# Performance work log

Hardware: AMD Instinct MI355X
Metric: run time of the kernel (lower is better)

## Reference

```python
import jax, jax.numpy as jnp
import numpy as np

EPS = 1e-5
HD = 16          # hidden_dim
OC = 256         # out_chs
NH = 8           # num_heads (groups of qkv conv)
DV = OC // (2 * HD)  # per-head value dim = 8


def conv_bn_silu(x, w, gamma, beta, mean, var, stride=1, pad=1, groups=1):
    # Conv2d(bias=False) + BatchNorm2d(eval) + SiLU, NCHW/OIHW
    y = jax.lax.conv_general_dilated(
        x, w, (stride, stride), [(pad, pad), (pad, pad)],
        dimension_numbers=('NCHW', 'OIHW', 'NCHW'),
        feature_group_count=groups)
    inv = gamma * jax.lax.rsqrt(var + EPS)
    y = y * inv[None, :, None, None] + (beta - mean * inv)[None, :, None, None]
    return y * jax.nn.sigmoid(y)


def _bn_params(key, c):
    k1, k2, k3, k4 = jax.random.split(key, 4)
    g = 1.0 + 0.1 * jax.random.normal(k1, (c,), jnp.float32)
    b = 0.1 * jax.random.normal(k2, (c,), jnp.float32)
    m = 0.1 * jax.random.normal(k3, (c,), jnp.float32)
    v = jax.random.uniform(k4, (c,), jnp.float32, 0.5, 1.5)
    return g, b, m, v


def setup_inputs() -> dict:
    key = jax.random.key(0)
    ks = jax.random.split(key, 8)
    B, C, H, W = 16, 256, 80, 80
    qkv_out = HD * 2 + OC // 2  # 160
    d = {}
    d['x'] = jax.random.normal(ks[0], (B, C, H, W), jnp.float32)
    # qkv_conv: grouped 3x3, groups=NH -> in per group = C//NH
    d['qkv_w'] = jax.random.normal(ks[1], (qkv_out, C // NH, 3, 3), jnp.float32) * 0.05
    d['qkv_g'], d['qkv_b'], d['qkv_m'], d['qkv_v'] = _bn_params(ks[2], qkv_out)
    # hidden_conv: dense 3x3
    d['hid_w'] = jax.random.normal(ks[3], (OC, C, 3, 3), jnp.float32) * 0.02
    d['hid_g'], d['hid_b'], d['hid_m'], d['hid_v'] = _bn_params(ks[4], OC)
    # out_conv: 1x1 on (OC//2*3) channels
    d['out_w'] = jax.random.normal(ks[5], (OC, OC // 2 * 3, 1, 1), jnp.float32) * 0.05
    d['out_g'], d['out_b'], d['out_m'], d['out_v'] = _bn_params(ks[6], OC)
    return d


def reference(x, qkv_w, qkv_g, qkv_b, qkv_m, qkv_v,
              hid_w, hid_g, hid_b, hid_m, hid_v,
              out_w, out_g, out_b, out_m, out_v):
    B, C, H, W = x.shape
    N = H * W
    qkv = conv_bn_silu(x, qkv_w, qkv_g, qkv_b, qkv_m, qkv_v, stride=1, pad=1, groups=NH)
    q = qkv[:, :HD]               # (B, HD, H, W)
    k = qkv[:, HD:2 * HD]
    v = qkv[:, 2 * HD:]           # (B, OC//2, H, W)
    # permute to (B, N, HD) / (B, N, HD, DV), channel-major reshape matches torch .view
    q = q.transpose(0, 2, 3, 1).reshape(B, N, HD)
    k = k.transpose(0, 2, 3, 1).reshape(B, N, HD)
    v = v.transpose(0, 2, 3, 1).reshape(B, N, HD, DV)
    # per-pixel tiny attention: attn[b,n,i,j] = softmax_j(q_i * k_j)
    attn = jax.nn.softmax(q[..., :, None] * k[..., None, :], axis=-1)  # (B,N,HD,HD)
    y = jnp.einsum('bnij,bnjd->bnid', attn, v)                          # (B,N,HD,DV)
    # torch: permute(0,2,3,1).view(B, OC//2, H, W)
    y = y.transpose(0, 2, 3, 1).reshape(B, OC // 2, H, W)
    h = conv_bn_silu(x, hid_w, hid_g, hid_b, hid_m, hid_v, stride=1, pad=1)
    y = jnp.concatenate([y, h], axis=1)  # (B, OC//2*3, H, W)
    return conv_bn_silu(y, out_w, out_g, out_b, out_m, out_v, stride=1, pad=0)
```

## Files before the change

kernel.cpp:

```cpp
#include <hip/hip_runtime.h>
#include <stdint.h>

typedef unsigned short u16;
typedef unsigned int u32;
typedef __attribute__((ext_vector_type(4))) float f32x4;
typedef __attribute__((ext_vector_type(8))) __bf16 bf16x8;

#define EPS_BN 1e-5f

__device__ __forceinline__ u16 f2bf(float f) {
  u32 u = __builtin_bit_cast(u32, f);
  u32 r = (u + 0x7fffu + ((u >> 16) & 1u)) >> 16;
  return (u16)r;
}

__device__ __forceinline__ float silu_f(float v) {
  return v / (1.0f + __expf(-v));
}

__device__ __forceinline__ void gll16(const void* g, void* l) {
  __builtin_amdgcn_global_load_lds(
      (__attribute__((address_space(1))) void*)(void*)g,
      (__attribute__((address_space(3))) void*)l, 16, 0, 0);
}

__global__ __launch_bounds__(256) void prep(
    const float* __restrict__ qkv_w, const float* __restrict__ qg,
    const float* __restrict__ qb, const float* __restrict__ qm,
    const float* __restrict__ qv,
    const float* __restrict__ hid_w, const float* __restrict__ hg,
    const float* __restrict__ hb, const float* __restrict__ hm,
    const float* __restrict__ hv,
    const float* __restrict__ out_w, const float* __restrict__ og,
    const float* __restrict__ ob, const float* __restrict__ om,
    const float* __restrict__ ov,
    u16* __restrict__ wtb, u16* __restrict__ w2b, u16* __restrict__ wqp,
    float* __restrict__ bnq_s, float* __restrict__ bnq_b,
    float* __restrict__ bnh_s, float* __restrict__ bnh_b,
    float* __restrict__ bn2s, float* __restrict__ bn2b,
    float* __restrict__ zpg)
{
  const int gid = blockIdx.x * 256 + threadIdx.x;
  if (gid < 256 * 2304) {
    int j = gid / 2304, k = gid - j * 2304;
    int tap = k >> 8, c = k & 255;
    wtb[gid] = f2bf(hid_w[(j * 256 + c) * 9 + tap]);
  }
  if (gid < 73728) {
    int g = gid / 9216;
    int r = gid - g * 9216;
    int j = r / 288, k = r - j * 288;
    int tap = k >> 5, cg = k & 31;
    float v = 0.f;
    if (j < 20) v = qkv_w[((g * 20 + j) * 32 + cg) * 9 + tap];
    wqp[gid] = f2bf(v);
  }
  if (gid < 98304) w2b[gid] = f2bf(out_w[gid]);
  if (gid < 160) {
    float iv = qg[gid] * rsqrtf(qv[gid] + EPS_BN);
    bnq_s[gid] = iv; bnq_b[gid] = qb[gid] - qm[gid] * iv;
  }
  if (gid < 256) {
    float iv = hg[gid] * rsqrtf(hv[gid] + EPS_BN);
    bnh_s[gid] = iv; bnh_b[gid] = hb[gid] - hm[gid] * iv;
    float iv2 = og[gid] * rsqrtf(ov[gid] + EPS_BN);
    bn2s[gid] = iv2; bn2b[gid] = ob[gid] - om[gid] * iv2;
  }
  if (gid < 64) zpg[gid] = 0.f;
}

__global__ __launch_bounds__(256) void nchw2nhwc(
    const float* __restrict__ x, u16* __restrict__ xn)
{
  __shared__ u16 T[80 * 66];
  const int t = threadIdx.x;
  const int ct = blockIdx.x;
  const int h  = blockIdx.y;
  const int b  = blockIdx.z;
  const float* src = x + ((size_t)b * 256 + ct * 64) * 6400 + h * 80;
  for (int it = 0; it < 5; ++it) {
    int idx = it * 256 + t;
    int cl = idx / 20, w4 = idx - cl * 20;
    float4 v = *(const float4*)(src + (size_t)cl * 6400 + w4 * 4);
    T[(w4 * 4 + 0) * 66 + cl] = f2bf(v.x);
    T[(w4 * 4 + 1) * 66 + cl] = f2bf(v.y);
    T[(w4 * 4 + 2) * 66 + cl] = f2bf(v.z);
    T[(w4 * 4 + 3) * 66 + cl] = f2bf(v.w);
  }
  __syncthreads();
  u16* dst = xn + ((size_t)(b * 80 + h) * 80) * 256 + ct * 64;
  for (int it = 0; it < 5; ++it) {
    int idx = it * 256 + t;
    int wl = idx >> 4;
    int cl = (idx & 15) * 4;
    ushort4 v4;
    v4.x = T[wl * 66 + cl + 0];
    v4.y = T[wl * 66 + cl + 1];
    v4.z = T[wl * 66 + cl + 2];
    v4.w = T[wl * 66 + cl + 3];
    *(ushort4*)(dst + (size_t)wl * 256 + cl) = v4;
  }
}

__global__ __launch_bounds__(256, 2) void gemm_main(
    const u16* __restrict__ xn, const u16* __restrict__ wt,
    const float* __restrict__ bns, const float* __restrict__ bnb,
    const float* __restrict__ zpg, u16* __restrict__ ycat)
{
  __shared__ __attribute__((aligned(16))) u16 Al[128 * 64];
  __shared__ __attribute__((aligned(16))) u16 Bl[128 * 64];
  const int t = threadIdx.x;
  const int wave = t >> 6, lane = t & 63;
  const int wr = wave >> 1, wc = wave & 1;
  const int orig = blockIdx.y * 2 + blockIdx.x;
  const int wg = (orig & 7) * 200 + (orig >> 3);
  const int jtile = (wg / 800) * 128;
  const int ptile = (wg % 800) * 128;

  const int srcc = (((lane & 7) ^ ((lane >> 3) & 7)) * 8);
  int pb[4], hh[4], wwv[4], bofB[4];
#pragma unroll
  for (int c = 0; c < 4; ++c) {
    int m = wave * 32 + c * 8 + (lane >> 3);
    int p = ptile + m;
    pb[c] = p;
    int hw = p % 6400;
    hh[c] = hw / 80;
    wwv[c] = hw - (hw / 80) * 80;
    bofB[c] = (jtile + m) * 2304 + srcc;
  }
  u16* AlW = Al + wave * 2048;
  u16* BlW = Bl + wave * 2048;

  f32x4 acc[4][4];
#pragma unroll
  for (int m = 0; m < 4; ++m)
#pragma unroll
    for (int n = 0; n < 4; ++n) {
      f32x4 z = {0.f, 0.f, 0.f, 0.f};
      acc[m][n] = z;
    }

  for (int ks = 0; ks < 36; ++ks) {
    const int k0 = ks * 64;
    const int tap = k0 >> 8;
    const int c0 = k0 & 255;
    const int dh = tap / 3 - 1, dw = tap - (tap / 3) * 3 - 1;
    __syncthreads();
#pragma unroll
    for (int c = 0; c < 4; ++c) {
      int h2 = hh[c] + dh, w2 = wwv[c] + dw;
      bool ok = ((unsigned)h2 < 80u) & ((unsigned)w2 < 80u);
      const u16* src = ok
          ? (xn + ((size_t)(pb[c] + dh * 80 + dw) * 256 + c0 + srcc))
          : (const u16*)zpg;
      gll16(src, AlW + c * 512);
    }
#pragma unroll
    for (int c = 0; c < 4; ++c)
      gll16(wt + (size_t)(bofB[c] + k0), BlW + c * 512);
    __syncthreads();
#pragma unroll
    for (int kk = 0; kk < 2; ++kk) {
      const int q = kk * 4 + (lane >> 4);
      const int c16 = lane & 15;
      bf16x8 av[4], bv[4];
#pragma unroll
      for (int m = 0; m < 4; ++m) {
        int r = wr * 64 + m * 16 + c16;
        av[m] = *(const bf16x8*)(Al + r * 64 + (q ^ (r & 7)) * 8);
      }
#pragma unroll
      for (int n = 0; n < 4; ++n) {
        int r = wc * 64 + n * 16 + c16;
        bv[n] = *(const bf16x8*)(Bl + r * 64 + (q ^ (r & 7)) * 8);
      }
#pragma unroll
      for (int m = 0; m < 4; ++m)
#pragma unroll
        for (int n = 0; n < 4; ++n)
          acc[m][n] = __builtin_amdgcn_mfma_f32_16x16x32_bf16(
              av[m], bv[n], acc[m][n], 0, 0, 0);
    }
  }

  const int c16 = lane & 15, rg = lane >> 4;
#pragma unroll
  for (int n = 0; n < 4; ++n) {
    int j = jtile + wc * 64 + n * 16 + c16;
    float sc = bns[j], bi = bnb[j];
#pragma unroll
    for (int m = 0; m < 4; ++m) {
      int p0 = ptile + wr * 64 + m * 16 + rg * 4;
#pragma unroll
      for (int r = 0; r < 4; ++r) {
        float v = silu_f(acc[m][n][r] * sc + bi);
        ycat[(size_t)(p0 + r) * 384 + 128 + j] = f2bf(v);
      }
    }
  }
}

__global__ __launch_bounds__(256, 2) void qkv_attn(
    const u16* __restrict__ xn, const u16* __restrict__ wqp,
    const float* __restrict__ bnq_s, const float* __restrict__ bnq_b,
    u16* __restrict__ ycat)
{
  __shared__ __attribute__((aligned(16))) char LB[81920];
  u16* HB0 = (u16*)LB;
  u16* HB1 = (u16*)(LB + 40960);
  float* qs = (float*)LB;

  const int t = threadIdx.x;
  const int wave = t >> 6, lane = t & 63;
  const int orig = blockIdx.x;
  const int wg = (orig & 7) * 100 + (orig >> 3);
  const int ptile = wg * 128;
  const int pbase = ptile - 88;

  const int srcc = (((lane & 7) ^ ((lane >> 3) & 7)) * 8);
  const int q = lane >> 4, c16 = lane & 15;

  int ph[2], pw[2];
#pragma unroll
  for (int m = 0; m < 2; ++m) {
    int p = ptile + wave * 32 + m * 16 + c16;
    int hw = p % 6400;
    ph[m] = hw / 80;
    pw[m] = hw - (hw / 80) * 80;
  }

  auto STAGE_H = [&](int cc, u16* dst) {
#pragma unroll
    for (int r = 0; r < 10; ++r) {
      int row = r * 32 + wave * 8 + (lane >> 3);
      int p = pbase + row;
      int pc = p < 0 ? 0 : (p > 102399 ? 102399 : p);
      gll16(xn + (size_t)pc * 256 + cc * 64 + srcc,
            dst + (r * 32 + wave * 8) * 64);
    }
  };

  bf16x8 zv;
#pragma unroll
  for (int i = 0; i < 8; ++i) zv[i] = (__bf16)0.0f;

  f32x4 acc[2][16];
#pragma unroll
  for (int m = 0; m < 2; ++m)
#pragma unroll
    for (int f = 0; f < 16; ++f) {
      f32x4 z = {0.f, 0.f, 0.f, 0.f};
      acc[m][f] = z;
    }

  STAGE_H(0, HB0);
  asm volatile("s_waitcnt vmcnt(0)" ::: "memory");
  __builtin_amdgcn_sched_barrier(0);
  __syncthreads();

#pragma unroll
  for (int cc = 0; cc < 4; ++cc) {
    const u16* HBc = (cc & 1) ? HB1 : HB0;
    u16* HBn = (cc & 1) ? HB0 : HB1;
    if (cc < 3) STAGE_H(cc + 1, HBn);
    for (int tap = 0; tap < 9; ++tap) {
      const int dh = tap / 3 - 1, dw = tap - (tap / 3) * 3 - 1;
      const int dp = dh * 80 + dw;
      bf16x8 bq[2][2];
#pragma unroll
      for (int h = 0; h < 2; ++h)
#pragma unroll
        for (int nf = 0; nf < 2; ++nf) {
          int row = (2 * cc + h) * 32 + nf * 16 + c16;
          bq[h][nf] =
              *(const bf16x8*)(wqp + (size_t)row * 288 + tap * 32 + q * 8);
        }
      bf16x8 av[2][2];
#pragma unroll
      for (int m = 0; m < 2; ++m) {
        int rl = wave * 32 + m * 16 + c16 + 88 + dp;
        bool ok = ((unsigned)(ph[m] + dh) < 80u) &
                  ((unsigned)(pw[m] + dw) < 80u);
#pragma unroll
        for (int h = 0; h < 2; ++h) {
          int q8 = h * 4 + q;
          bf16x8 raw = *(const bf16x8*)(HBc + rl * 64 + ((q8 ^ (rl & 7)) * 8));
          av[m][h] = ok ? raw : zv;
        }
      }
#pragma unroll
      for (int h = 0; h < 2; ++h)
#pragma unroll
        for (int m = 0; m < 2; ++m)
#pragma unroll
          for (int nf = 0; nf < 2; ++nf)
            acc[m][(2 * cc + h) * 2 + nf] = __builtin_amdgcn_mfma_f32_16x16x32_bf16(
                av[m][h], bq[h][nf], acc[m][(2 * cc + h) * 2 + nf], 0, 0, 0);
    }
    if (cc < 3) {
      asm volatile("s_waitcnt vmcnt(0)" ::: "memory");
      __builtin_amdgcn_sched_barrier(0);
      __syncthreads();
    }
  }

  asm volatile("s_waitcnt vmcnt(0)" ::: "memory");
  __builtin_amdgcn_sched_barrier(0);
  __syncthreads();

#pragma unroll
  for (int f = 0; f < 16; ++f) {
    int jj = (f & 1) * 16 + c16;
    if (jj >= 20) continue;
    int oc = (f >> 1) * 20 + jj;
    float sc = bnq_s[oc], bi = bnq_b[oc];
#pragma unroll
    for (int m = 0; m < 2; ++m) {
      int pl0 = wave * 32 + m * 16 + q * 4;
#pragma unroll
      for (int r = 0; r < 4; ++r)
        qs[(pl0 + r) * 160 + oc] = silu_f(acc[m][f][r] * sc + bi);
    }
  }
  __syncthreads();

  for (int it = 0; it < 8; ++it) {
    int idx = it * 256 + t;
    int px = idx >> 4, i = idx & 15;
    const float* row = qs + px * 160;
    const float qi = row[i];
    float s[16];
    float mx = -3.4e38f;
#pragma unroll
    for (int j = 0; j < 16; ++j) { s[j] = qi * row[16 + j]; mx = fmaxf(mx, s[j]); }
    float sum = 0.f;
#pragma unroll
    for (int j = 0; j < 16; ++j) { s[j] = __expf(s[j] - mx); sum += s[j]; }
    const float inv = 1.0f / sum;
    float y[8];
#pragma unroll
    for (int d = 0; d < 8; ++d) y[d] = 0.f;
#pragma unroll
    for (int j = 0; j < 16; ++j) {
      const float a = s[j];
      const float* vr = row + 32 + j * 8;
#pragma unroll
      for (int d = 0; d < 8; ++d) y[d] += a * vr[d];
    }
    union { u16 u[8]; uint4 v4; } pk;
#pragma unroll
    for (int d = 0; d < 8; ++d) pk.u[d] = f2bf(y[d] * inv);
    *(uint4*)(ycat + (size_t)(ptile + px) * 384 + i * 8) = pk.v4;
  }
}

__global__ __launch_bounds__(256, 2) void gemm_out(
    const u16* __restrict__ w2, const u16* __restrict__ ycat,
    const float* __restrict__ bns, const float* __restrict__ bnb,
    float* __restrict__ out)
{
  __shared__ __attribute__((aligned(16))) u16 Al[128 * 64];
  __shared__ __attribute__((aligned(16))) u16 Bl[128 * 64];
  const int t = threadIdx.x;
  const int wave = t >> 6, lane = t & 63;
  const int wr = wave >> 1, wc = wave & 1;
  const int orig = blockIdx.y * 2 + blockIdx.x;
  const int wg = (orig & 7) * 200 + (orig >> 3);
  const int octile = (wg / 800) * 128;
  const int ptile = (wg % 800) * 128;

  const int srcc = (((lane & 7) ^ ((lane >> 3) & 7)) * 8);
  int bofA[4], bofB[4];
#pragma unroll
  for (int c = 0; c < 4; ++c) {
    int m = wave * 32 + c * 8 + (lane >> 3);
    bofA[c] = (octile + m) * 384 + srcc;
    bofB[c] = (ptile + m) * 384 + srcc;
  }
  u16* AlW = Al + wave * 2048;
  u16* BlW = Bl + wave * 2048;

  f32x4 acc[4][4];
#pragma unroll
  for (int m = 0; m < 4; ++m)
#pragma unroll
    for (int n = 0; n < 4; ++n) {
      f32x4 z = {0.f, 0.f, 0.f, 0.f};
      acc[m][n] = z;
    }

  for (int ks = 0; ks < 6; ++ks) {
    const int k0 = ks * 64;
    __syncthreads();
#pragma unroll
    for (int c = 0; c < 4; ++c) gll16(w2 + (size_t)(bofA[c] + k0), AlW + c * 512);
#pragma unroll
    for (int c = 0; c < 4; ++c) gll16(ycat + (size_t)(bofB[c] + k0), BlW + c * 512);
    __syncthreads();
#pragma unroll
    for (int kk = 0; kk < 2; ++kk) {
      const int q = kk * 4 + (lane >> 4);
      const int c16 = lane & 15;
      bf16x8 av[4], bv[4];
#pragma unroll
      for (int m = 0; m < 4; ++m) {
        int r = wr * 64 + m * 16 + c16;
        av[m] = *(const bf16x8*)(Al + r * 64 + (q ^ (r & 7)) * 8);
      }
#pragma unroll
      for (int n = 0; n < 4; ++n) {
        int r = wc * 64 + n * 16 + c16;
        bv[n] = *(const bf16x8*)(Bl + r * 64 + (q ^ (r & 7)) * 8);
      }
#pragma unroll
      for (int m = 0; m < 4; ++m)
#pragma unroll
        for (int n = 0; n < 4; ++n)
          acc[m][n] = __builtin_amdgcn_mfma_f32_16x16x32_bf16(
              av[m], bv[n], acc[m][n], 0, 0, 0);
    }
  }

  const int c16 = lane & 15, rg = lane >> 4;
  const int b = ptile / 6400;
  const int hwb = ptile - b * 6400;
#pragma unroll
  for (int m = 0; m < 4; ++m) {
    int oc0 = octile + wr * 64 + m * 16 + rg * 4;
#pragma unroll
    for (int n = 0; n < 4; ++n) {
      int hw = hwb + wc * 64 + n * 16 + c16;
#pragma unroll
      for (int r = 0; r < 4; ++r) {
        int oc = oc0 + r;
        float v = silu_f(acc[m][n][r] * bns[oc] + bnb[oc]);
        out[((size_t)b * 256 + oc) * 6400 + hw] = v;
      }
    }
  }
}

extern "C" void kernel_launch(void* const* d_in, const int* in_sizes, int n_in,
                              void* d_out, int out_size, void* d_ws, size_t ws_size,
                              hipStream_t stream) {
  (void)in_sizes; (void)n_in; (void)out_size; (void)ws_size;
  const float* x    = (const float*)d_in[0];
  const float* qkvw = (const float*)d_in[1];
  const float* qg   = (const float*)d_in[2];
  const float* qb   = (const float*)d_in[3];
  const float* qm   = (const float*)d_in[4];
  const float* qv   = (const float*)d_in[5];
  const float* hw_  = (const float*)d_in[6];
  const float* hg   = (const float*)d_in[7];
  const float* hb   = (const float*)d_in[8];
  const float* hm   = (const float*)d_in[9];
  const float* hv   = (const float*)d_in[10];
  const float* ow   = (const float*)d_in[11];
  const float* og   = (const float*)d_in[12];
  const float* ob   = (const float*)d_in[13];
  const float* om   = (const float*)d_in[14];
  const float* ov   = (const float*)d_in[15];

  char* ws = (char*)d_ws;
  float* zpg   = (float*)(ws + 0);
  float* bnq_s = (float*)(ws + 256);
  float* bnq_b = (float*)(ws + 1280);
  float* bnh_s = (float*)(ws + 2304);
  float* bnh_b = (float*)(ws + 3328);
  float* bn2s  = (float*)(ws + 4352);
  float* bn2b  = (float*)(ws + 5376);
  u16*   wtb   = (u16*)(ws + 6400);
  u16*   w2b   = (u16*)(ws + 1186048);
  u16*   wqp   = (u16*)(ws + 1382656);
  u16*   xn    = (u16*)(ws + 1536000);
  u16*   ycat  = (u16*)(ws + 119500800);
  float* out   = (float*)d_out;

  prep<<<dim3(2304), dim3(256), 0, stream>>>(
      qkvw, qg, qb, qm, qv, hw_, hg, hb, hm, hv, ow, og, ob, om, ov,
      wtb, w2b, wqp, bnq_s, bnq_b, bnh_s, bnh_b, bn2s, bn2b, zpg);
  nchw2nhwc<<<dim3(4, 80, 16), dim3(256), 0, stream>>>(x, xn);
  gemm_main<<<dim3(2, 800), dim3(256), 0, stream>>>(
      xn, wtb, bnh_s, bnh_b, zpg, ycat);
  qkv_attn<<<dim3(800), dim3(256), 0, stream>>>(
      xn, wqp, bnq_s, bnq_b, ycat);
  gemm_out<<<dim3(2, 800), dim3(256), 0, stream>>>(
      w2b, ycat, bn2s, bn2b, out);
}
```

Before: 314.5 us.

## Widen GEMM tiles to cover all 256 output channels per 512-thread block

Both gemm_main and gemm_out now use 512-thread blocks with 8 waves. Each block computes a 128-pixel by 256-channel tile instead of two separate 128x128 tiles, so the im2col activation tile (gemm_main) or the ycat tile (gemm_out) is loaded once per pixel tile rather than twice. The cost is larger LDS use (48KB per block), larger blocks, and a different occupancy point; the launch bounds request 4 blocks of 512 threads.

```diff
diff --git a/kernel.cpp b/kernel.cpp
--- a/kernel.cpp
+++ b/kernel.cpp
@@ -102,35 +102,40 @@
   }
 }
 
-__global__ __launch_bounds__(256, 2) void gemm_main(
+__global__ __launch_bounds__(512, 4) void gemm_main(
     const u16* __restrict__ xn, const u16* __restrict__ wt,
     const float* __restrict__ bns, const float* __restrict__ bnb,
     const float* __restrict__ zpg, u16* __restrict__ ycat)
 {
   __shared__ __attribute__((aligned(16))) u16 Al[128 * 64];
-  __shared__ __attribute__((aligned(16))) u16 Bl[128 * 64];
+  __shared__ __attribute__((aligned(16))) u16 Bl[256 * 64];
   const int t = threadIdx.x;
   const int wave = t >> 6, lane = t & 63;
-  const int wr = wave >> 1, wc = wave & 1;
-  const int orig = blockIdx.y * 2 + blockIdx.x;
-  const int wg = (orig & 7) * 200 + (orig >> 3);
-  const int jtile = (wg / 800) * 128;
-  const int ptile = (wg % 800) * 128;
+  const int wm = wave >> 2;
+  const int wn = wave & 3;
+  const int orig = blockIdx.x;
+  const int wg = (orig & 7) * 100 + (orig >> 3);
+  const int ptile = wg * 128;
 
   const int srcc = (((lane & 7) ^ ((lane >> 3) & 7)) * 8);
-  int pb[4], hh[4], wwv[4], bofB[4];
-#pragma unroll
-  for (int c = 0; c < 4; ++c) {
-    int m = wave * 32 + c * 8 + (lane >> 3);
-    int p = ptile + m;
-    pb[c] = p;
+  const int c16 = lane & 15, lq = lane >> 4;
+
+  int pbA[2], hhA[2], wwA[2];
+#pragma unroll
+  for (int l = 0; l < 2; ++l) {
+    int row = wave * 8 + (lane >> 3) + l * 64;
+    int p = ptile + row;
+    pbA[l] = p;
     int hw = p % 6400;
-    hh[c] = hw / 80;
-    wwv[c] = hw - (hw / 80) * 80;
-    bofB[c] = (jtile + m) * 2304 + srcc;
-  }
-  u16* AlW = Al + wave * 2048;
-  u16* BlW = Bl + wave * 2048;
+    hhA[l] = hw / 80;
+    wwA[l] = hw - (hw / 80) * 80;
+  }
+  int bofB[4];
+#pragma unroll
+  for (int l = 0; l < 4; ++l) {
+    int row = wave * 8 + (lane >> 3) + l * 64;
+    bofB[l] = row * 2304 + srcc;
+  }
 
   f32x4 acc[4][4];
 #pragma unroll
@@ -143,37 +148,36 @@
 
   for (int ks = 0; ks < 36; ++ks) {
     const int k0 = ks * 64;
-    const int tap = k0 >> 8;
-    const int c0 = k0 & 255;
+    const int tap = ks >> 2;
+    const int c0 = (ks & 3) * 64;
     const int dh = tap / 3 - 1, dw = tap - (tap / 3) * 3 - 1;
+    const int dp = dh * 80 + dw;
     __syncthreads();
 #pragma unroll
-    for (int c = 0; c < 4; ++c) {
-      int h2 = hh[c] + dh, w2 = wwv[c] + dw;
-      bool ok = ((unsigned)h2 < 80u) & ((unsigned)w2 < 80u);
+    for (int l = 0; l < 2; ++l) {
+      bool ok = ((unsigned)(hhA[l] + dh) < 80u) & ((unsigned)(wwA[l] + dw) < 80u);
       const u16* src = ok
-          ? (xn + ((size_t)(pb[c] + dh * 80 + dw) * 256 + c0 + srcc))
+          ? (xn + ((size_t)(pbA[l] + dp) * 256 + c0 + srcc))
           : (const u16*)zpg;
-      gll16(src, AlW + c * 512);
-    }
-#pragma unroll
-    for (int c = 0; c < 4; ++c)
-      gll16(wt + (size_t)(bofB[c] + k0), BlW + c * 512);
+      gll16(src, Al + (wave * 8 + l * 64) * 64);
+    }
+#pragma unroll
+    for (int l = 0; l < 4; ++l)
+      gll16(wt + (size_t)(bofB[l] + k0), Bl + (wave * 8 + l * 64) * 64);
     __syncthreads();
 #pragma unroll
     for (int kk = 0; kk < 2; ++kk) {
-      const int q = kk * 4 + (lane >> 4);
-      const int c16 = lane & 15;
+      const int q = kk * 4 + lq;
       bf16x8 av[4], bv[4];
 #pragma unroll
       for (int m = 0; m < 4; ++m) {
-        int r = wr * 64 + m * 16 + c16;
+        int r = wm * 64 + m * 16 + c16;
         av[m] = *(const bf16x8*)(Al + r * 64 + (q ^ (r & 7)) * 8);
       }
 #pragma unroll
       for (int n = 0; n < 4; ++n) {
-        int r = wc * 64 + n * 16 + c16;
-        bv[n] = *(const bf16x8*)(Bl + r * 64 + (q ^ (r & 7)) * 8);
+        int j = wn * 64 + n * 16 + c16;
+        bv[n] = *(const bf16x8*)(Bl + j * 64 + (q ^ (j & 7)) * 8);
       }
 #pragma unroll
       for (int m = 0; m < 4; ++m)
@@ -184,14 +188,14 @@
     }
   }
 
-  const int c16 = lane & 15, rg = lane >> 4;
+  const int rg = lq;
 #pragma unroll
   for (int n = 0; n < 4; ++n) {
-    int j = jtile + wc * 64 + n * 16 + c16;
+    int j = wn * 64 + n * 16 + c16;
     float sc = bns[j], bi = bnb[j];
 #pragma unroll
     for (int m = 0; m < 4; ++m) {
-      int p0 = ptile + wr * 64 + m * 16 + rg * 4;
+      int p0 = ptile + wm * 64 + m * 16 + rg * 4;
 #pragma unroll
       for (int r = 0; r < 4; ++r) {
         float v = silu_f(acc[m][n][r] * sc + bi);
@@ -355,31 +359,35 @@
   }
 }
 
-__global__ __launch_bounds__(256, 2) void gemm_out(
+__global__ __launch_bounds__(512, 4) void gemm_out(
     const u16* __restrict__ w2, const u16* __restrict__ ycat,
     const float* __restrict__ bns, const float* __restrict__ bnb,
     float* __restrict__ out)
 {
-  __shared__ __attribute__((aligned(16))) u16 Al[128 * 64];
+  __shared__ __attribute__((aligned(16))) u16 Al[256 * 64];
   __shared__ __attribute__((aligned(16))) u16 Bl[128 * 64];
   const int t = threadIdx.x;
   const int wave = t >> 6, lane = t & 63;
-  const int wr = wave >> 1, wc = wave & 1;
-  const int orig = blockIdx.y * 2 + blockIdx.x;
-  const int wg = (orig & 7) * 200 + (orig >> 3);
-  const int octile = (wg / 800) * 128;
-  const int ptile = (wg % 800) * 128;
+  const int wm = wave >> 1;
+  const int wn = wave & 1;
+  const int orig = blockIdx.x;
+  const int wg = (orig & 7) * 100 + (orig >> 3);
+  const int ptile = wg * 128;
 
   const int srcc = (((lane & 7) ^ ((lane >> 3) & 7)) * 8);
-  int bofA[4], bofB[4];
-#pragma unroll
-  for (int c = 0; c < 4; ++c) {
-    int m = wave * 32 + c * 8 + (lane >> 3);
-    bofA[c] = (octile + m) * 384 + srcc;
-    bofB[c] = (ptile + m) * 384 + srcc;
-  }
-  u16* AlW = Al + wave * 2048;
-  u16* BlW = Bl + wave * 2048;
+  const int c16 = lane & 15, lq = lane >> 4;
+
+  int bofA[4], bofB[2];
+#pragma unroll
+  for (int l = 0; l < 4; ++l) {
+    int row = wave * 8 + (lane >> 3) + l * 64;
+    bofA[l] = row * 384 + srcc;
+  }
+#pragma unroll
+  for (int l = 0; l < 2; ++l) {
+    int row = wave * 8 + (lane >> 3) + l * 64;
+    bofB[l] = (ptile + row) * 384 + srcc;
+  }
 
   f32x4 acc[4][4];
 #pragma unroll
@@ -394,24 +402,25 @@
     const int k0 = ks * 64;
     __syncthreads();
 #pragma unroll
-    for (int c = 0; c < 4; ++c) gll16(w2 + (size_t)(bofA[c] + k0), AlW + c * 512);
-#pragma unroll
-    for (int c = 0; c < 4; ++c) gll16(ycat + (size_t)(bofB[c] + k0), BlW + c * 512);
+    for (int l = 0; l < 4; ++l)
+      gll16(w2 + (size_t)(bofA[l] + k0), Al + (wave * 8 + l * 64) * 64);
+#pragma unroll
+    for (int l = 0; l < 2; ++l)
+      gll16(ycat + (size_t)(bofB[l] + k0), Bl + (wave * 8 + l * 64) * 64);
     __syncthreads();
 #pragma unroll
     for (int kk = 0; kk < 2; ++kk) {
-      const int q = kk * 4 + (lane >> 4);
-      const int c16 = lane & 15;
+      const int q = kk * 4 + lq;
       bf16x8 av[4], bv[4];
 #pragma unroll
       for (int m = 0; m < 4; ++m) {
-        int r = wr * 64 + m * 16 + c16;
+        int r = wm * 64 + m * 16 + c16;
         av[m] = *(const bf16x8*)(Al + r * 64 + (q ^ (r & 7)) * 8);
       }
 #pragma unroll
       for (int n = 0; n < 4; ++n) {
-        int r = wc * 64 + n * 16 + c16;
-        bv[n] = *(const bf16x8*)(Bl + r * 64 + (q ^ (r & 7)) * 8);
+        int j = wn * 64 + n * 16 + c16;
+        bv[n] = *(const bf16x8*)(Bl + j * 64 + (q ^ (j & 7)) * 8);
       }
 #pragma unroll
       for (int m = 0; m < 4; ++m)
@@ -422,15 +431,15 @@
     }
   }
 
-  const int c16 = lane & 15, rg = lane >> 4;
+  const int rg = lq;
   const int b = ptile / 6400;
   const int hwb = ptile - b * 6400;
 #pragma unroll
   for (int m = 0; m < 4; ++m) {
-    int oc0 = octile + wr * 64 + m * 16 + rg * 4;
+    int oc0 = wm * 64 + m * 16 + rg * 4;
 #pragma unroll
     for (int n = 0; n < 4; ++n) {
-      int hw = hwb + wc * 64 + n * 16 + c16;
+      int hw = hwb + wn * 64 + n * 16 + c16;
 #pragma unroll
       for (int r = 0; r < 4; ++r) {
         int oc = oc0 + r;
@@ -481,10 +490,10 @@
       qkvw, qg, qb, qm, qv, hw_, hg, hb, hm, hv, ow, og, ob, om, ov,
       wtb, w2b, wqp, bnq_s, bnq_b, bnh_s, bnh_b, bn2s, bn2b, zpg);
   nchw2nhwc<<<dim3(4, 80, 16), dim3(256), 0, stream>>>(x, xn);
-  gemm_main<<<dim3(2, 800), dim3(256), 0, stream>>>(
+  gemm_main<<<dim3(800), dim3(512), 0, stream>>>(
       xn, wtb, bnh_s, bnh_b, zpg, ycat);
   qkv_attn<<<dim3(800), dim3(256), 0, stream>>>(
       xn, wqp, bnq_s, bnq_b, ycat);
-  gemm_out<<<dim3(2, 800), dim3(256), 0, stream>>>(
+  gemm_out<<<dim3(800), dim3(512), 0, stream>>>(
       w2b, ycat, bn2s, bn2b, out);
 }
```

After: 313.2 us. Within noise of the previous version (-0.4%).
